# Optimization experiments

Measured on AMD Instinct MI355X. Metric: run time of the kernel, lower is better.

The kernel has to match this reference:

```python
import jax, jax.numpy as jnp
import numpy as np

EPS = 1e-6

def _ln(x, g, b):
    # channels-first LayerNorm over C (per-pixel), matching custom LayerNorm in repo
    m = jnp.mean(x, 1, keepdims=True)
    v = jnp.mean((x - m) ** 2, 1, keepdims=True)
    return (x - m) * jax.lax.rsqrt(v + EPS) * g[None, :, None, None] + b[None, :, None, None]

def _c1(x, w, b=None):
    y = jnp.einsum('oc,bchw->bohw', w, x)
    return y if b is None else y + b[None, :, None, None]

def _dw(x, w, b=None, pad=1, dil=1):
    y = jax.lax.conv_general_dilated(x, w, (1, 1), [(pad, pad), (pad, pad)],
                                     rhs_dilation=(dil, dil), feature_group_count=x.shape[1],
                                     dimension_numbers=('NCHW', 'OIHW', 'NCHW'))
    return y if b is None else y + b[None, :, None, None]

def _dwt_haar(x):
    # single-level 2D haar DWT (zero mode, even H/W so no padding needed)
    a = x[:, :, 0::2, 0::2]; b = x[:, :, 0::2, 1::2]
    c = x[:, :, 1::2, 0::2]; d = x[:, :, 1::2, 1::2]
    ll = (a + b + c + d) * 0.5
    hl = (b - a + d - c) * 0.5
    lh = (c - a + d - b) * 0.5
    hh = (a - b - c + d) * 0.5
    return ll, hl, lh, hh

def _ss2d(x, xp, dtw, dtb, alog, dp):
    # 4-direction Mamba-style selective scan (VMamba SS2D core)
    B, D, H, W = x.shape
    L = H * W; K = 4; R = dtw.shape[-1]; N = alog.shape[-1]
    x1 = x.reshape(B, D, L)                                   # row-major scan
    x2 = jnp.transpose(x, (0, 1, 3, 2)).reshape(B, D, L)      # col-major scan
    xs = jnp.stack([x1, x2], 1)
    xs = jnp.concatenate([xs, jnp.flip(xs, -1)], 1)           # (B,4,D,L)
    xdbl = jnp.einsum('bkdl,kcd->bkcl', xs, xp)               # (B,4,R+2N,L)
    dts, Bs, Cs = jnp.split(xdbl, [R, R + N], axis=2)
    dts = jax.nn.softplus(jnp.einsum('bkrl,kdr->bkdl', dts, dtw) + dtb[None, :, :, None])
    A = -jnp.exp(alog)                                        # (K,D,N)

    def step(h, inp):
        u, dt, Bt, Ct = inp
        h = h * jnp.exp(dt[..., None] * A) + (dt * u)[..., None] * Bt[:, :, None, :]
        return h, jnp.einsum('bkdn,bkn->bkd', h, Ct)

    h0 = jnp.zeros((B, K, D, N), x.dtype)
    _, ys = jax.lax.scan(step, h0, (jnp.moveaxis(xs, -1, 0), jnp.moveaxis(dts, -1, 0),
                                    jnp.moveaxis(Bs, -1, 0), jnp.moveaxis(Cs, -1, 0)))
    y = jnp.moveaxis(ys, 0, -1) + dp[None, :, :, None] * xs   # (B,4,D,L)

    def wh(z):
        return jnp.transpose(z.reshape(B, D, W, H), (0, 1, 3, 2)).reshape(B, D, L)

    out = y[:, 0] + jnp.flip(y[:, 2], -1) + wh(y[:, 1]) + wh(jnp.flip(y[:, 3], -1))
    return out.reshape(B, D, H, W)

def forward(x, wt_dw, wt_db, wt_lng, wt_lnb, wt_ctw, wt_ctb,
            cv_inw, cv_ln1g, cv_ln1b, cv_pw, cv_dww, cv_dwb,
            ss_xp, ss_dtw, ss_dtb, ss_alog, ss_d,
            cv_ong, cv_onb, cv_ow, cv_skip, eca_w, wgm_skip,
            pf_nw, pf_nb, pf_lng, pf_lnb, pf_d1, pf_d2, pf_d3, pf_d4,
            pf_flng, pf_flnb, pf_fw, pf_fb, pf_skip):
    # ---- WT_Block ----
    q = _ln(_c1(x, wt_dw, wt_db), wt_lng, wt_lnb)
    ll, hl, lh, hh = _dwt_haar(q)
    q = jnp.concatenate([ll, hl, lh, hh], 1)                  # (B,C,H/2,W/2)
    # ConvTranspose2d(k=2, s=2): out[2i+p,2j+q] = sum_c in[i,j] * W[c,o,p,q]
    y = jnp.einsum('bcij,copq->boipjq', q, wt_ctw)
    Bq, Co, Hh, _, Ww, _ = y.shape
    q = y.reshape(Bq, Co, 2 * Hh, 2 * Ww) + wt_ctb[None, :, None, None]
    # ---- CVSS_Block ----
    h = _ln(_c1(q, cv_inw), cv_ln1g, cv_ln1b)
    skip_in = h
    h = _c1(h, cv_pw)
    h = jax.nn.silu(_dw(h, cv_dww, cv_dwb, pad=1))
    h = _ss2d(h, ss_xp, ss_dtw, ss_dtb, ss_alog, ss_d)
    h = _ln(h, cv_ong, cv_onb)
    q = _c1(h, cv_ow) + skip_in * cv_skip
    # ---- ECA ----
    v = jnp.mean(q, (2, 3))[:, None, :]                       # (B,1,C)
    v = jax.lax.conv_general_dilated(v, eca_w, (1,), [(1, 1)],
                                     dimension_numbers=('NCH', 'OIH', 'NCH'))
    v = jax.nn.sigmoid(v)[:, 0, :, None, None]
    x = v * q + wgm_skip * x
    # ---- PF_Block ----
    res = _ln(_c1(x, pf_nw, pf_nb), pf_lng, pf_lnb)
    x1, x2, x3, x4 = jnp.split(res, 4, axis=1)
    x1 = _dw(x1, pf_d1, pad=1)
    x2 = _dw(x1 + x2, pf_d2, pad=3)
    x3 = _dw(x2 + x3, pf_d3, pad=2, dil=2)
    x4 = _dw(x3 + x4, pf_d4, pad=3, dil=3)
    cat = jnp.concatenate([x1, x2, x3, x4], 1)
    return jax.nn.silu(_c1(_ln(cat, pf_flng, pf_flnb), pf_fw, pf_fb)) + pf_skip * res

def setup_inputs() -> dict:
    key = jax.random.key(0)
    C, B, H, W = 64, 4, 64, 64
    N, R, D2, K, C4 = 16, 4, 2 * C, 4, C // 4
    ks = jax.random.split(key, 20)
    def rn(i, shape, s):
        return jax.random.normal(ks[i], shape, jnp.float32) * s
    inp = {}
    inp['x'] = jax.random.normal(ks[0], (B, C, H, W), jnp.float32)
    inp['wt_dw'] = rn(1, (C4, C), 0.1); inp['wt_db'] = jnp.zeros((C4,))
    inp['wt_lng'] = jnp.ones((C4,)); inp['wt_lnb'] = jnp.zeros((C4,))
    inp['wt_ctw'] = rn(2, (C, C, 2, 2), 0.1); inp['wt_ctb'] = jnp.zeros((C,))
    inp['cv_inw'] = rn(3, (C, C), 0.1)
    inp['cv_ln1g'] = jnp.ones((C,)); inp['cv_ln1b'] = jnp.zeros((C,))
    inp['cv_pw'] = rn(4, (D2, C), 0.1)
    inp['cv_dww'] = rn(5, (D2, 1, 3, 3), 0.2); inp['cv_dwb'] = jnp.zeros((D2,))
    inp['ss_xp'] = rn(6, (K, R + 2 * N, D2), 0.05)
    inp['ss_dtw'] = rn(7, (K, D2, R), 0.1)
    inp['ss_dtb'] = jnp.full((K, D2), -4.0) + rn(8, (K, D2), 0.1)
    inp['ss_alog'] = jnp.tile(jnp.log(jnp.arange(1.0, N + 1.0, dtype=jnp.float32)), (K, D2, 1))
    inp['ss_d'] = jnp.ones((K, D2))
    inp['cv_ong'] = jnp.ones((D2,)); inp['cv_onb'] = jnp.zeros((D2,))
    inp['cv_ow'] = rn(9, (C, D2), 0.1); inp['cv_skip'] = jnp.ones((1,))
    inp['eca_w'] = rn(10, (1, 1, 3), 0.5)
    inp['wgm_skip'] = jnp.ones((1,))
    inp['pf_nw'] = rn(11, (C, C), 0.1); inp['pf_nb'] = jnp.zeros((C,))
    inp['pf_lng'] = jnp.ones((C,)); inp['pf_lnb'] = jnp.zeros((C,))
    inp['pf_d1'] = rn(12, (C4, 1, 3, 3), 0.2)
    inp['pf_d2'] = rn(13, (C4, 1, 7, 7), 0.1)
    inp['pf_d3'] = rn(14, (C4, 1, 3, 3), 0.2)
    inp['pf_d4'] = rn(15, (C4, 1, 3, 3), 0.2)
    inp['pf_flng'] = jnp.ones((C,)); inp['pf_flnb'] = jnp.zeros((C,))
    inp['pf_fw'] = rn(16, (C, C), 0.1); inp['pf_fb'] = jnp.zeros((C,))
    inp['pf_skip'] = jnp.ones((1,))
    return inp

def reference(x, wt_dw, wt_db, wt_lng, wt_lnb, wt_ctw, wt_ctb,
              cv_inw, cv_ln1g, cv_ln1b, cv_pw, cv_dww, cv_dwb,
              ss_xp, ss_dtw, ss_dtb, ss_alog, ss_d,
              cv_ong, cv_onb, cv_ow, cv_skip, eca_w, wgm_skip,
              pf_nw, pf_nb, pf_lng, pf_lnb, pf_d1, pf_d2, pf_d3, pf_d4,
              pf_flng, pf_flnb, pf_fw, pf_fb, pf_skip):
    return forward(x, wt_dw, wt_db, wt_lng, wt_lnb, wt_ctw, wt_ctb,
                   cv_inw, cv_ln1g, cv_ln1b, cv_pw, cv_dww, cv_dwb,
                   ss_xp, ss_dtw, ss_dtb, ss_alog, ss_d,
                   cv_ong, cv_onb, cv_ow, cv_skip, eca_w, wgm_skip,
                   pf_nw, pf_nb, pf_lng, pf_lnb, pf_d1, pf_d2, pf_d3, pf_d4,
                   pf_flng, pf_flnb, pf_fw, pf_fb, pf_skip)
```

## Files before the change

kernel.cpp:

```cpp
#include <hip/hip_runtime.h>
#include <cstdint>
#include <cstddef>

#define B_ 4
#define C_ 64
#define C4_ 16
#define D_ 128
#define H_ 64
#define W_ 64
#define L_ 4096
#define K_ 4
#define N_ 16
#define R_ 4
#define NC_ 64
#define CL_ 64
#define EPS_ 1e-6f

#define DEV __device__ __forceinline__

DEV float sigmoidf_(float x){ return 1.f/(1.f+__expf(-x)); }
DEV float siluf_(float x){ return x*sigmoidf_(x); }
DEV float softplusf_(float x){ return fmaxf(x,0.f) + __logf(1.f+__expf(-fabsf(x))); }

__global__ __launch_bounds__(64) void k1_inln(
    const float* __restrict__ x, const float* __restrict__ w,
    const float* __restrict__ bias, const float* __restrict__ g,
    const float* __restrict__ bb, float* __restrict__ q1)
{
  int t = blockIdx.x*64 + threadIdx.x;
  int b = t >> 12; int pix = t & (L_-1);
  const float* xb = x + (size_t)b*C_*L_ + pix;
  float acc[C4_];
  #pragma unroll
  for(int o=0;o<C4_;o++) acc[o] = bias[o];
  for(int c=0;c<C_;c++){
    float xv = xb[(size_t)c*L_];
    #pragma unroll
    for(int o=0;o<C4_;o++) acc[o] = fmaf(w[o*C_+c], xv, acc[o]);
  }
  float m=0.f;
  #pragma unroll
  for(int o=0;o<C4_;o++) m += acc[o];
  m *= (1.f/C4_);
  float var=0.f;
  #pragma unroll
  for(int o=0;o<C4_;o++){ float d=acc[o]-m; var += d*d; }
  var *= (1.f/C4_);
  float rs = rsqrtf(var+EPS_);
  float* qb = q1 + (size_t)b*C4_*L_ + pix;
  #pragma unroll
  for(int o=0;o<C4_;o++) qb[(size_t)o*L_] = (acc[o]-m)*rs*g[o] + bb[o];
}

__global__ __launch_bounds__(256) void k2a_dwtct(
    const float* __restrict__ q1, const float* __restrict__ ctw,
    const float* __restrict__ ctb, float* __restrict__ q2)
{
  int t = blockIdx.x*256 + threadIdx.x;
  int pix = t & (L_-1);
  int bq = t >> 12; int b = bq >> 2; int quarter = bq & 3;
  int y = pix >> 6, xw = pix & 63;
  int i = y >> 1, p = y & 1, j = xw >> 1, q = xw & 1;
  const float* qb = q1 + (size_t)b*C4_*L_;
  int p00 = (2*i)*W_ + 2*j;
  float ll[16], hl[16], lh[16], hh[16];
  #pragma unroll
  for(int c=0;c<16;c++){
    const float* pc = qb + (size_t)c*L_ + p00;
    float a = pc[0], bb2 = pc[1], cc = pc[W_], dd = pc[W_+1];
    ll[c] = (a+bb2+cc+dd)*0.5f;
    hl[c] = (bb2-a+dd-cc)*0.5f;
    lh[c] = (cc-a+dd-bb2)*0.5f;
    hh[c] = (a-bb2-cc+dd)*0.5f;
  }
  int pq = p*2+q;
  int obase = quarter*16;
  float* q2b = q2 + (size_t)b*C_*L_ + pix;
  #pragma unroll
  for(int oo=0;oo<16;oo++){
    int o = obase+oo;
    float acc = ctb[o];
    const float* wb = ctw + o*4 + pq;
    #pragma unroll
    for(int c=0;c<16;c++){
      acc = fmaf(ll[c], wb[c*256],       acc);
      acc = fmaf(hl[c], wb[(16+c)*256],  acc);
      acc = fmaf(lh[c], wb[(32+c)*256],  acc);
      acc = fmaf(hh[c], wb[(48+c)*256],  acc);
    }
    q2b[(size_t)o*L_] = acc;
  }
}

__global__ __launch_bounds__(64) void k2b_inconv_ln(
    const float* __restrict__ q2, const float* __restrict__ w,
    const float* __restrict__ g, const float* __restrict__ bb,
    float* __restrict__ skip)
{
  int t = blockIdx.x*64 + threadIdx.x;
  int b = t >> 12; int pix = t & (L_-1);
  const float* qb = q2 + (size_t)b*C_*L_ + pix;
  float acc[C_];
  #pragma unroll
  for(int o=0;o<C_;o++) acc[o]=0.f;
  for(int c=0;c<C_;c++){
    float xv = qb[(size_t)c*L_];
    #pragma unroll
    for(int o=0;o<C_;o++) acc[o] = fmaf(w[o*C_+c], xv, acc[o]);
  }
  float m=0.f;
  #pragma unroll
  for(int o=0;o<C_;o++) m += acc[o];
  m *= (1.f/C_);
  float var=0.f;
  #pragma unroll
  for(int o=0;o<C_;o++){ float d=acc[o]-m; var += d*d; }
  var *= (1.f/C_);
  float rs = rsqrtf(var+EPS_);
  float* sb = skip + (size_t)b*C_*L_ + pix;
  #pragma unroll
  for(int o=0;o<C_;o++) sb[(size_t)o*L_] = (acc[o]-m)*rs*g[o] + bb[o];
}

__global__ __launch_bounds__(256) void k3_pw(
    const float* __restrict__ skip, const float* __restrict__ w,
    float* __restrict__ hp)
{
  int t = blockIdx.x*256 + threadIdx.x;
  int pix = t & (L_-1);
  int bg = t >> 12; int b = bg >> 3; int grp = bg & 7;
  const float* sb = skip + (size_t)b*C_*L_ + pix;
  float acc[16];
  #pragma unroll
  for(int o=0;o<16;o++) acc[o]=0.f;
  for(int c=0;c<C_;c++){
    float xv = sb[(size_t)c*L_];
    #pragma unroll
    for(int oo=0;oo<16;oo++) acc[oo]=fmaf(w[(grp*16+oo)*C_+c], xv, acc[oo]);
  }
  float* hb = hp + (size_t)b*D_*L_ + (size_t)(grp*16)*L_ + pix;
  #pragma unroll
  for(int oo=0;oo<16;oo++) hb[(size_t)oo*L_] = acc[oo];
}

__global__ __launch_bounds__(256) void k4_dwsilu(
    const float* __restrict__ hp, const float* __restrict__ wdw,
    const float* __restrict__ bdw, float* __restrict__ hd,
    float* __restrict__ hdt)
{
  __shared__ float tin[64][65];
  __shared__ float tout[64][65];
  int bc = blockIdx.x;
  int ch = bc & (D_-1);
  const float* plane = hp + (size_t)bc*L_;
  int tid = threadIdx.x;
  #pragma unroll
  for(int qq=0;qq<16;qq++){ int lin = tid + qq*256; tin[lin>>6][lin&63] = plane[lin]; }
  __syncthreads();
  float wv[9];
  #pragma unroll
  for(int i=0;i<9;i++) wv[i] = wdw[ch*9+i];
  float bv = bdw[ch];
  float* hdp = hd + (size_t)bc*L_;
  #pragma unroll
  for(int qq=0;qq<16;qq++){
    int lin = tid + qq*256; int h = lin>>6, w = lin&63;
    float acc = bv;
    #pragma unroll
    for(int ky=0;ky<3;ky++){
      int hh = h+ky-1; if(hh<0||hh>=64) continue;
      #pragma unroll
      for(int kx=0;kx<3;kx++){
        int ww = w+kx-1; if(ww<0||ww>=64) continue;
        acc = fmaf(wv[ky*3+kx], tin[hh][ww], acc);
      }
    }
    float s = siluf_(acc);
    hdp[lin] = s;
    tout[h][w] = s;
  }
  __syncthreads();
  float* hdtp = hdt + (size_t)bc*L_;
  #pragma unroll
  for(int qq=0;qq<16;qq++){
    int lin = tid + qq*256;
    hdtp[lin] = tout[lin&63][lin>>6];
  }
}

__global__ __launch_bounds__(256) void k5_proj(
    const float* __restrict__ hd, const float* __restrict__ hdt,
    const float* __restrict__ xp, float* __restrict__ xd4,
    float* __restrict__ bsb, float* __restrict__ csb)
{
  int l = blockIdx.x*256 + threadIdx.x;
  int k = blockIdx.y, b = blockIdx.z;
  int pixv = (k<2)? l : (L_-1-l);
  const float* src = ((k&1)? hdt : hd) + (size_t)b*D_*L_ + pixv;
  const float* xpk = xp + k*36*D_;
  float xd[36];
  #pragma unroll
  for(int c=0;c<36;c++) xd[c]=0.f;
  for(int d=0;d<D_;d++){
    float u = src[(size_t)d*L_];
    #pragma unroll
    for(int c=0;c<36;c++) xd[c] = fmaf(xpk[c*D_+d], u, xd[c]);
  }
  int bk = b*K_+k;
  float4* xq = (float4*)(xd4 + ((size_t)bk*L_ + l)*4);
  *xq = make_float4(xd[0], xd[1], xd[2], xd[3]);
  float* bp = bsb + ((size_t)bk*L_ + l)*N_;
  float* cp = csb + ((size_t)bk*L_ + l)*N_;
  #pragma unroll
  for(int n=0;n<N_;n++){ bp[n]=xd[4+n]; cp[n]=xd[20+n]; }
}


__global__ __launch_bounds__(128) void k6_scan1(
    const float* __restrict__ xd4, const float* __restrict__ hd,
    const float* __restrict__ hdt, const float* __restrict__ bsb,
    const float* __restrict__ dtw, const float* __restrict__ dtb,
    const float* __restrict__ alog, float* __restrict__ ca, float* __restrict__ cb)
{
  __shared__ float su[128][65];
  __shared__ float4 sb4[64][4];
  __shared__ float4 sx[64];
  int chunk = blockIdx.x, k = blockIdx.y, b = blockIdx.z;
  int d = threadIdx.x;
  int bk = b*K_ + k;
  bool rev = (k >= 2);
  int base_l = rev ? (63-chunk)*CL_ : chunk*CL_;
  const float* src = ((k&1)? hdt : hd) + (size_t)b*D_*L_;
  #pragma unroll
  for(int p=0;p<16;p++){
    int idx = p*128 + d; int row = idx >> 4, c4 = idx & 15;
    float4 v = *(const float4*)(src + (size_t)row*L_ + base_l + c4*4);
    su[row][c4*4+0]=v.x; su[row][c4*4+1]=v.y; su[row][c4*4+2]=v.z; su[row][c4*4+3]=v.w;
  }
  const float4* bsrc = (const float4*)(bsb + ((size_t)bk*L_ + chunk*CL_)*N_);
  #pragma unroll
  for(int p=0;p<2;p++){
    int idx = p*128 + d; int row = idx>>2, q = idx&3;
    sb4[row][q] = bsrc[idx];
  }
  {
    const float4* xsrc = (const float4*)(xd4 + ((size_t)bk*L_ + chunk*CL_)*4);
    if(d < 64) sx[d] = xsrc[d];
  }
  float A[N_];
  {
    const float* al = alog + ((size_t)k*D_+d)*N_;
    #pragma unroll
    for(int n=0;n<N_;n++) A[n] = -__expf(al[n]);
  }
  float4 wv = *(const float4*)(dtw + ((size_t)k*D_+d)*R_);
  float bdt = dtb[k*D_+d];
  __syncthreads();
  float h[N_];
  #pragma unroll
  for(int n=0;n<N_;n++) h[n]=0.f;
  float S=0.f;
  for(int i=0;i<CL_;i++){
    int jj = rev ? (CL_-1-i) : i;
    float4 xv = sx[i];
    float r = fmaf(xv.x,wv.x, fmaf(xv.y,wv.y, fmaf(xv.z,wv.z, fmaf(xv.w,wv.w, bdt))));
    float dt = softplusf_(r);
    float u = su[d][jj];
    S += dt;
    float du = dt*u;
    #pragma unroll
    for(int n4=0;n4<4;n4++){
      float4 bv = sb4[i][n4];
      int n0=n4*4;
      h[n0+0] = fmaf(du, bv.x, h[n0+0]*__expf(dt*A[n0+0]));
      h[n0+1] = fmaf(du, bv.y, h[n0+1]*__expf(dt*A[n0+1]));
      h[n0+2] = fmaf(du, bv.z, h[n0+2]*__expf(dt*A[n0+2]));
      h[n0+3] = fmaf(du, bv.w, h[n0+3]*__expf(dt*A[n0+3]));
    }
  }
  size_t obase = (((size_t)bk*NC_ + chunk)*D_ + d)*N_;
  float4* cap = (float4*)(ca + obase);
  float4* cbp = (float4*)(cb + obase);
  #pragma unroll
  for(int n4=0;n4<4;n4++){
    int n0=n4*4;
    cap[n4] = make_float4(__expf(S*A[n0]), __expf(S*A[n0+1]), __expf(S*A[n0+2]), __expf(S*A[n0+3]));
    cbp[n4] = make_float4(h[n0], h[n0+1], h[n0+2], h[n0+3]);
  }
}

__global__ __launch_bounds__(256) void k7_scan2(
    const float* __restrict__ ca, const float* __restrict__ cb,
    float* __restrict__ h0)
{
  int t = blockIdx.x*256 + threadIdx.x;
  int bk = t >> 11; int dn = t & 2047;
  size_t base = (size_t)bk*NC_*D_*N_ + dn;
  float h=0.f;
  for(int c=0;c<NC_;c++){
    size_t idx = base + (size_t)c*D_*N_;
    h0[idx] = h;
    h = fmaf(ca[idx], h, cb[idx]);
  }
}

__global__ __launch_bounds__(128) void k8_scan3(
    const float* __restrict__ xd4, const float* __restrict__ hd,
    const float* __restrict__ hdt, const float* __restrict__ bsb,
    const float* __restrict__ csb, const float* __restrict__ h0b,
    const float* __restrict__ dtw, const float* __restrict__ dtb,
    const float* __restrict__ alog, const float* __restrict__ dp,
    float* __restrict__ ys)
{
  __shared__ float su[128][65];
  __shared__ float4 sb4[64][4];
  __shared__ float4 sc4[64][4];
  __shared__ float4 sx[64];
  int chunk = blockIdx.x, k = blockIdx.y, b = blockIdx.z;
  int d = threadIdx.x;
  int bk = b*K_ + k;
  bool rev = (k >= 2);
  int base_l = rev ? (63-chunk)*CL_ : chunk*CL_;
  const float* src = ((k&1)? hdt : hd) + (size_t)b*D_*L_;
  #pragma unroll
  for(int p=0;p<16;p++){
    int idx = p*128 + d; int row = idx >> 4, c4 = idx & 15;
    float4 v = *(const float4*)(src + (size_t)row*L_ + base_l + c4*4);
    su[row][c4*4+0]=v.x; su[row][c4*4+1]=v.y; su[row][c4*4+2]=v.z; su[row][c4*4+3]=v.w;
  }
  const float4* bsrc = (const float4*)(bsb + ((size_t)bk*L_ + chunk*CL_)*N_);
  const float4* csrc = (const float4*)(csb + ((size_t)bk*L_ + chunk*CL_)*N_);
  #pragma unroll
  for(int p=0;p<2;p++){
    int idx = p*128 + d; int row = idx>>2, q = idx&3;
    sb4[row][q] = bsrc[idx];
    sc4[row][q] = csrc[idx];
  }
  {
    const float4* xsrc = (const float4*)(xd4 + ((size_t)bk*L_ + chunk*CL_)*4);
    if(d < 64) sx[d] = xsrc[d];
  }
  float A[N_];
  {
    const float* al = alog + ((size_t)k*D_+d)*N_;
    #pragma unroll
    for(int n=0;n<N_;n++) A[n] = -__expf(al[n]);
  }
  float4 wv = *(const float4*)(dtw + ((size_t)k*D_+d)*R_);
  float bdt = dtb[k*D_+d];
  float dpv = dp[k*D_+d];
  float h[N_];
  {
    size_t hbase = (((size_t)bk*NC_ + chunk)*D_ + d)*N_;
    const float4* h4 = (const float4*)(h0b + hbase);
    #pragma unroll
    for(int n4=0;n4<4;n4++){
      float4 hv = h4[n4];
      h[n4*4+0]=hv.x; h[n4*4+1]=hv.y; h[n4*4+2]=hv.z; h[n4*4+3]=hv.w;
    }
  }
  __syncthreads();
  for(int i=0;i<CL_;i++){
    int jj = rev ? (CL_-1-i) : i;
    float4 xv = sx[i];
    float r = fmaf(xv.x,wv.x, fmaf(xv.y,wv.y, fmaf(xv.z,wv.z, fmaf(xv.w,wv.w, bdt))));
    float dt = softplusf_(r);
    float u = su[d][jj];
    float du = dt*u;
    float y = 0.f;
    #pragma unroll
    for(int n4=0;n4<4;n4++){
      float4 bv = sb4[i][n4];
      float4 cv = sc4[i][n4];
      int n0=n4*4;
      h[n0+0] = fmaf(du, bv.x, h[n0+0]*__expf(dt*A[n0+0])); y = fmaf(h[n0+0], cv.x, y);
      h[n0+1] = fmaf(du, bv.y, h[n0+1]*__expf(dt*A[n0+1])); y = fmaf(h[n0+1], cv.y, y);
      h[n0+2] = fmaf(du, bv.z, h[n0+2]*__expf(dt*A[n0+2])); y = fmaf(h[n0+2], cv.z, y);
      h[n0+3] = fmaf(du, bv.w, h[n0+3]*__expf(dt*A[n0+3])); y = fmaf(h[n0+3], cv.w, y);
    }
    y = fmaf(dpv, u, y);
    su[d][jj] = y;
  }
  __syncthreads();
  #pragma unroll
  for(int p=0;p<16;p++){
    int idx = p*128 + d; int row = idx >> 4, c4 = idx & 15;
    int m0 = c4*4;
    float4 v;
    if(rev) v = make_float4(su[row][63-m0], su[row][62-m0], su[row][61-m0], su[row][60-m0]);
    else    v = make_float4(su[row][m0], su[row][m0+1], su[row][m0+2], su[row][m0+3]);
    *(float4*)(ys + ((size_t)bk*D_ + row)*L_ + chunk*CL_ + m0) = v;
  }
}

__global__ __launch_bounds__(256) void k9t_comb(
    const float* __restrict__ ys, float* __restrict__ yc)
{
  __shared__ float t1[64][65];
  __shared__ float t3[64][65];
  int bd = blockIdx.x; int b = bd >> 7; int d = bd & (D_-1);
  const float* y0 = ys + ((size_t)(b*K_+0)*D_ + d)*L_;
  const float* y1 = ys + ((size_t)(b*K_+1)*D_ + d)*L_;
  const float* y2 = ys + ((size_t)(b*K_+2)*D_ + d)*L_;
  const float* y3 = ys + ((size_t)(b*K_+3)*D_ + d)*L_;
  int tid = threadIdx.x;
  #pragma unroll
  for(int qq=0;qq<16;qq++){
    int lin = tid + qq*256;
    t1[lin>>6][lin&63] = y1[lin];
    t3[lin>>6][lin&63] = y3[lin];
  }
  __syncthreads();
  float* outp = yc + ((size_t)b*D_ + d)*L_;
  #pragma unroll
  for(int qq=0;qq<16;qq++){
    int lin = tid + qq*256; int h = lin>>6, w = lin&63;
    outp[lin] = y0[lin] + t1[w][h] + y2[L_-1-lin] + t3[63-w][63-h];
  }
}

__global__ __launch_bounds__(256) void k9a_ln(
    const float* __restrict__ yc, const float* __restrict__ g,
    const float* __restrict__ bb, float* __restrict__ hn)
{
  __shared__ float ssum[4][64];
  __shared__ float ssq[4][64];
  int tid = threadIdx.x;
  int pl = tid & 63;
  int wg = tid >> 6;
  int t = blockIdx.x*64 + pl;
  int b = t >> 12; int pix = t & (L_-1);
  const float* ybase = yc + (size_t)b*D_*L_ + (size_t)(wg*32)*L_ + pix;
  float v[32];
  float s = 0.f;
  #pragma unroll
  for(int i=0;i<32;i++){ v[i] = ybase[(size_t)i*L_]; s += v[i]; }
  ssum[wg][pl] = s;
  __syncthreads();
  float S = ssum[0][pl]+ssum[1][pl]+ssum[2][pl]+ssum[3][pl];
  float m = S*(1.f/D_);
  float vq = 0.f;
  #pragma unroll
  for(int i=0;i<32;i++){ float dv = v[i]-m; vq = fmaf(dv,dv,vq); }
  ssq[wg][pl] = vq;
  __syncthreads();
  float VQ = ssq[0][pl]+ssq[1][pl]+ssq[2][pl]+ssq[3][pl];
  float rs = rsqrtf(VQ*(1.f/D_)+EPS_);
  float* hb = hn + (size_t)b*D_*L_ + (size_t)(wg*32)*L_ + pix;
  #pragma unroll
  for(int i=0;i<32;i++) hb[(size_t)i*L_] = (v[i]-m)*rs*g[wg*32+i] + bb[wg*32+i];
}

__global__ __launch_bounds__(256) void k9b_ow(
    const float* __restrict__ hn, const float* __restrict__ w,
    const float* __restrict__ skip, const float* __restrict__ cskip,
    float* __restrict__ qg, float* __restrict__ meansum)
{
  int t = blockIdx.x*256 + threadIdx.x;
  int pix = t & (L_-1); int bg = t >> 12; int b = bg >> 2; int grp = bg & 3;
  const float* hb = hn + (size_t)b*D_*L_ + pix;
  float acc[16];
  #pragma unroll
  for(int o=0;o<16;o++) acc[o]=0.f;
  for(int dd=0;dd<D_;dd++){
    float xv = hb[(size_t)dd*L_];
    #pragma unroll
    for(int oo=0;oo<16;oo++) acc[oo]=fmaf(w[(grp*16+oo)*D_+dd], xv, acc[oo]);
  }
  float csk = cskip[0];
  const float* sb = skip + (size_t)b*C_*L_ + pix;
  float* qb = qg + (size_t)b*C_*L_ + pix;
  #pragma unroll
  for(int oo=0;oo<16;oo++){
    int o = grp*16+oo;
    float v = acc[oo] + csk*sb[(size_t)o*L_];
    qb[(size_t)o*L_] = v;
    acc[oo] = v;
  }
  #pragma unroll
  for(int oo=0;oo<16;oo++){
    float v = acc[oo];
    #pragma unroll
    for(int off=32;off>0;off>>=1) v += __shfl_down(v, off, 64);
    if((threadIdx.x & 63)==0) atomicAdd(&meansum[b*C_ + grp*16+oo], v);
  }
}

__global__ __launch_bounds__(256) void k10_eca(
    const float* __restrict__ meansum, const float* __restrict__ ew,
    float* __restrict__ vsig)
{
  int t = threadIdx.x; if(t >= B_*C_) return;
  int b=t>>6, c=t&63;
  const float sc = 1.f/(float)L_;
  float ml = (c>0)?  meansum[b*C_+c-1]*sc : 0.f;
  float mc =         meansum[b*C_+c]*sc;
  float mr = (c<63)? meansum[b*C_+c+1]*sc : 0.f;
  float r = ew[0]*ml + ew[1]*mc + ew[2]*mr;
  vsig[t] = sigmoidf_(r);
}

__global__ __launch_bounds__(64) void k11_res(
    const float* __restrict__ qg, const float* __restrict__ xin,
    const float* __restrict__ vsig, const float* __restrict__ wgm,
    const float* __restrict__ w, const float* __restrict__ nb,
    const float* __restrict__ g, const float* __restrict__ bb,
    float* __restrict__ res)
{
  int t = blockIdx.x*64 + threadIdx.x;
  int b = t >> 12, pix = t & (L_-1);
  float wg = wgm[0];
  const float* qb = qg + (size_t)b*C_*L_ + pix;
  const float* xb = xin + (size_t)b*C_*L_ + pix;
  float acc[C_];
  #pragma unroll
  for(int o=0;o<C_;o++) acc[o]=nb[o];
  for(int c=0;c<C_;c++){
    float x2 = vsig[b*C_+c]*qb[(size_t)c*L_] + wg*xb[(size_t)c*L_];
    #pragma unroll
    for(int o=0;o<C_;o++) acc[o] = fmaf(w[o*C_+c], x2, acc[o]);
  }
  float m=0.f;
  #pragma unroll
  for(int o=0;o<C_;o++) m += acc[o];
  m *= (1.f/C_);
  float var=0.f;
  #pragma unroll
  for(int o=0;o<C_;o++){ float d=acc[o]-m; var += d*d; }
  var *= (1.f/C_);
  float rs = rsqrtf(var+EPS_);
  float* rb = res + (size_t)b*C_*L_ + pix;
  #pragma unroll
  for(int o=0;o<C_;o++) rb[(size_t)o*L_] = (acc[o]-m)*rs*g[o] + bb[o];
}

DEV void conv_step(const float (*tin)[65], float (*tout)[65],
                   const float* __restrict__ wp, int ks, int pad, int dil,
                   float* __restrict__ gout, int tid)
{
  for(int qq=0;qq<16;qq++){
    int lin=tid+qq*256; int h=lin>>6, w=lin&63;
    float acc=0.f;
    for(int ky=0;ky<ks;ky++){
      int hh=h+ky*dil-pad; if(hh<0||hh>=64) continue;
      for(int kx=0;kx<ks;kx++){
        int ww=w+kx*dil-pad; if(ww<0||ww>=64) continue;
        acc = fmaf(wp[ky*ks+kx], tin[hh][ww], acc);
      }
    }
    tout[h][w]=acc; gout[lin]=acc;
  }
}

__global__ __launch_bounds__(256) void k12_cascade(
    const float* __restrict__ res, const float* __restrict__ d1,
    const float* __restrict__ d2, const float* __restrict__ d3,
    const float* __restrict__ d4, float* __restrict__ cat)
{
  __shared__ float ta[64][65];
  __shared__ float tb[64][65];
  int bc = blockIdx.x; int b = bc>>4; int c = bc&15;
  int tid = threadIdx.x;
  const float* rb = res + (size_t)b*C_*L_;
  float* catb = cat + (size_t)b*C_*L_;
  for(int qq=0;qq<16;qq++){ int lin=tid+qq*256; ta[lin>>6][lin&63] = rb[(size_t)c*L_+lin]; }
  __syncthreads();
  conv_step(ta, tb, d1+c*9, 3, 1, 1, catb + (size_t)c*L_, tid);
  __syncthreads();
  for(int qq=0;qq<16;qq++){ int lin=tid+qq*256; ta[lin>>6][lin&63] = tb[lin>>6][lin&63] + rb[(size_t)(16+c)*L_+lin]; }
  __syncthreads();
  conv_step(ta, tb, d2+c*49, 7, 3, 1, catb + (size_t)(16+c)*L_, tid);
  __syncthreads();
  for(int qq=0;qq<16;qq++){ int lin=tid+qq*256; ta[lin>>6][lin&63] = tb[lin>>6][lin&63] + rb[(size_t)(32+c)*L_+lin]; }
  __syncthreads();
  conv_step(ta, tb, d3+c*9, 3, 2, 2, catb + (size_t)(32+c)*L_, tid);
  __syncthreads();
  for(int qq=0;qq<16;qq++){ int lin=tid+qq*256; ta[lin>>6][lin&63] = tb[lin>>6][lin&63] + rb[(size_t)(48+c)*L_+lin]; }
  __syncthreads();
  conv_step(ta, tb, d4+c*9, 3, 3, 3, catb + (size_t)(48+c)*L_, tid);
}

__global__ __launch_bounds__(64) void k13_final(
    const float* __restrict__ cat, const float* __restrict__ res,
    const float* __restrict__ g, const float* __restrict__ bb,
    const float* __restrict__ fw, const float* __restrict__ fb,
    const float* __restrict__ pskip, float* __restrict__ out)
{
  int t = blockIdx.x*64 + threadIdx.x;
  int b = t >> 12, pix = t & (L_-1);
  const float* catb = cat + (size_t)b*C_*L_ + pix;
  float s=0.f;
  for(int c=0;c<C_;c++) s += catb[(size_t)c*L_];
  float m = s*(1.f/C_);
  float var=0.f;
  for(int c=0;c<C_;c++){ float d=catb[(size_t)c*L_]-m; var += d*d; }
  var *= (1.f/C_);
  float rs = rsqrtf(var+EPS_);
  float acc[C_];
  #pragma unroll
  for(int o=0;o<C_;o++) acc[o]=fb[o];
  for(int c=0;c<C_;c++){
    float cv = (catb[(size_t)c*L_]-m)*rs*g[c]+bb[c];
    #pragma unroll
    for(int o=0;o<C_;o++) acc[o] = fmaf(fw[o*C_+c], cv, acc[o]);
  }
  float ps = pskip[0];
  const float* rb = res + (size_t)b*C_*L_ + pix;
  float* ob = out + (size_t)b*C_*L_ + pix;
  #pragma unroll
  for(int o=0;o<C_;o++) ob[(size_t)o*L_] = siluf_(acc[o]) + ps*rb[(size_t)o*L_];
}

extern "C" void kernel_launch(void* const* d_in, const int* in_sizes, int n_in,
                              void* d_out, int out_size, void* d_ws, size_t ws_size,
                              hipStream_t stream)
{
  const float* x       = (const float*)d_in[0];
  const float* wt_dw   = (const float*)d_in[1];
  const float* wt_db   = (const float*)d_in[2];
  const float* wt_lng  = (const float*)d_in[3];
  const float* wt_lnb  = (const float*)d_in[4];
  const float* wt_ctw  = (const float*)d_in[5];
  const float* wt_ctb  = (const float*)d_in[6];
  const float* cv_inw  = (const float*)d_in[7];
  const float* cv_ln1g = (const float*)d_in[8];
  const float* cv_ln1b = (const float*)d_in[9];
  const float* cv_pw   = (const float*)d_in[10];
  const float* cv_dww  = (const float*)d_in[11];
  const float* cv_dwb  = (const float*)d_in[12];
  const float* ss_xp   = (const float*)d_in[13];
  const float* ss_dtw  = (const float*)d_in[14];
  const float* ss_dtb  = (const float*)d_in[15];
  const float* ss_alog = (const float*)d_in[16];
  const float* ss_d    = (const float*)d_in[17];
  const float* cv_ong  = (const float*)d_in[18];
  const float* cv_onb  = (const float*)d_in[19];
  const float* cv_ow   = (const float*)d_in[20];
  const float* cv_skip = (const float*)d_in[21];
  const float* eca_w   = (const float*)d_in[22];
  const float* wgm_skip= (const float*)d_in[23];
  const float* pf_nw   = (const float*)d_in[24];
  const float* pf_nb   = (const float*)d_in[25];
  const float* pf_lng  = (const float*)d_in[26];
  const float* pf_lnb  = (const float*)d_in[27];
  const float* pf_d1   = (const float*)d_in[28];
  const float* pf_d2   = (const float*)d_in[29];
  const float* pf_d3   = (const float*)d_in[30];
  const float* pf_d4   = (const float*)d_in[31];
  const float* pf_flng = (const float*)d_in[32];
  const float* pf_flnb = (const float*)d_in[33];
  const float* pf_fw   = (const float*)d_in[34];
  const float* pf_fb   = (const float*)d_in[35];
  const float* pf_skip = (const float*)d_in[36];
  float* outp = (float*)d_out;

  float* ws = (float*)d_ws;
  size_t off = 0;
  float* q1   = ws+off; off += (size_t)B_*C4_*L_;
  float* q2   = ws+off;
  float* qg   = q2;
  off += (size_t)B_*C_*L_;
  float* skip = ws+off; off += (size_t)B_*C_*L_;
  float* hp   = ws+off;
  float* ca   = hp;
  off += (size_t)B_*D_*L_;
  float* hd   = ws+off;
  float* res  = hd;
  off += (size_t)B_*D_*L_;
  float* hdt  = ws+off;
  float* cat  = hdt;
  off += (size_t)B_*D_*L_;
  float* xd4  = ws+off; off += (size_t)B_*K_*L_*R_;
  float* bs   = ws+off; off += (size_t)B_*K_*L_*N_;
  float* cs   = ws+off; off += (size_t)B_*K_*L_*N_;
  float* cb   = ws+off;
  float* hn   = cb;
  off += (size_t)B_*K_*D_*NC_*N_;
  float* h0   = ws+off;
  float* yc   = h0;
  off += (size_t)B_*K_*D_*NC_*N_;
  float* ys   = ws+off; off += (size_t)B_*K_*D_*L_;
  float* meansum = ws+off; off += 256;
  float* vsig    = ws+off; off += 256;
  (void)ws_size; (void)in_sizes; (void)n_in; (void)out_size;

  hipMemsetAsync(meansum, 0, B_*C_*sizeof(float), stream);

  k1_inln   <<<256, 64, 0, stream>>>(x, wt_dw, wt_db, wt_lng, wt_lnb, q1);
  k2a_dwtct <<<256, 256, 0, stream>>>(q1, wt_ctw, wt_ctb, q2);
  k2b_inconv_ln<<<256, 64, 0, stream>>>(q2, cv_inw, cv_ln1g, cv_ln1b, skip);
  k3_pw     <<<512, 256, 0, stream>>>(skip, cv_pw, hp);
  k4_dwsilu <<<512, 256, 0, stream>>>(hp, cv_dww, cv_dwb, hd, hdt);
  k5_proj   <<<dim3(16,4,4), 256, 0, stream>>>(hd, hdt, ss_xp, xd4, bs, cs);
  k6_scan1  <<<dim3(NC_,K_,B_), 128, 0, stream>>>(xd4, hd, hdt, bs, ss_dtw, ss_dtb, ss_alog, ca, cb);
  k7_scan2  <<<128, 256, 0, stream>>>(ca, cb, h0);
  k8_scan3  <<<dim3(NC_,K_,B_), 128, 0, stream>>>(xd4, hd, hdt, bs, cs, h0, ss_dtw, ss_dtb, ss_alog, ss_d, ys);
  k9t_comb  <<<512, 256, 0, stream>>>(ys, yc);
  k9a_ln    <<<256, 256, 0, stream>>>(yc, cv_ong, cv_onb, hn);
  k9b_ow    <<<256, 256, 0, stream>>>(hn, cv_ow, skip, cv_skip, qg, meansum);
  k10_eca   <<<1,   256, 0, stream>>>(meansum, eca_w, vsig);
  k11_res   <<<256, 64, 0, stream>>>(qg, x, vsig, wgm_skip, pf_nw, pf_nb, pf_lng, pf_lnb, res);
  k12_cascade<<<64, 256, 0, stream>>>(res, pf_d1, pf_d2, pf_d3, pf_d4, cat);
  k13_final <<<256, 64, 0, stream>>>(cat, res, pf_flng, pf_flnb, pf_fw, pf_fb, pf_skip, outp);
}
```

Before: 614.0 us.

## Split 64-channel pointwise+LN kernels across 4 warps and stage DWT weights in LDS

```diff
diff --git a/kernel.cpp b/kernel.cpp
--- a/kernel.cpp
+++ b/kernel.cpp
@@ -56,70 +56,90 @@
     const float* __restrict__ q1, const float* __restrict__ ctw,
     const float* __restrict__ ctb, float* __restrict__ q2)
 {
-  int t = blockIdx.x*256 + threadIdx.x;
-  int pix = t & (L_-1);
-  int bq = t >> 12; int b = bq >> 2; int quarter = bq & 3;
+  __shared__ float wl[4][64][16];
+  int blk = blockIdx.x;
+  int bq = blk >> 4; int b = bq >> 2; int quarter = bq & 3;
+  int tid = threadIdx.x;
+  #pragma unroll
+  for(int pp=0;pp<16;pp++){
+    int v = pp*256 + tid;
+    int pq = v >> 10; int c = (v >> 4) & 63; int o = v & 15;
+    wl[pq][c][o] = ctw[c*256 + (quarter*16+o)*4 + pq];
+  }
+  __syncthreads();
+  int pix = ((blk & 15) << 8) + tid;
   int y = pix >> 6, xw = pix & 63;
   int i = y >> 1, p = y & 1, j = xw >> 1, q = xw & 1;
+  int pq = p*2+q;
   const float* qb = q1 + (size_t)b*C4_*L_;
   int p00 = (2*i)*W_ + 2*j;
-  float ll[16], hl[16], lh[16], hh[16];
+  float acc[16];
+  #pragma unroll
+  for(int oo=0;oo<16;oo++) acc[oo] = ctb[quarter*16+oo];
   #pragma unroll
   for(int c=0;c<16;c++){
     const float* pc = qb + (size_t)c*L_ + p00;
     float a = pc[0], bb2 = pc[1], cc = pc[W_], dd = pc[W_+1];
-    ll[c] = (a+bb2+cc+dd)*0.5f;
-    hl[c] = (bb2-a+dd-cc)*0.5f;
-    lh[c] = (cc-a+dd-bb2)*0.5f;
-    hh[c] = (a-bb2-cc+dd)*0.5f;
-  }
-  int pq = p*2+q;
-  int obase = quarter*16;
-  float* q2b = q2 + (size_t)b*C_*L_ + pix;
-  #pragma unroll
-  for(int oo=0;oo<16;oo++){
-    int o = obase+oo;
-    float acc = ctb[o];
-    const float* wb = ctw + o*4 + pq;
-    #pragma unroll
-    for(int c=0;c<16;c++){
-      acc = fmaf(ll[c], wb[c*256],       acc);
-      acc = fmaf(hl[c], wb[(16+c)*256],  acc);
-      acc = fmaf(lh[c], wb[(32+c)*256],  acc);
-      acc = fmaf(hh[c], wb[(48+c)*256],  acc);
+    float ll = (a+bb2+cc+dd)*0.5f;
+    float hl = (bb2-a+dd-cc)*0.5f;
+    float lh = (cc-a+dd-bb2)*0.5f;
+    float hh = (a-bb2-cc+dd)*0.5f;
+    const float4* wll = (const float4*)&wl[pq][c][0];
+    const float4* whl = (const float4*)&wl[pq][16+c][0];
+    const float4* wlh = (const float4*)&wl[pq][32+c][0];
+    const float4* whh = (const float4*)&wl[pq][48+c][0];
+    #pragma unroll
+    for(int o4=0;o4<4;o4++){
+      float4 w0 = wll[o4], w1 = whl[o4], w2 = wlh[o4], w3 = whh[o4];
+      int o0 = o4*4;
+      acc[o0+0] = fmaf(ll,w0.x, fmaf(hl,w1.x, fmaf(lh,w2.x, fmaf(hh,w3.x, acc[o0+0]))));
+      acc[o0+1] = fmaf(ll,w0.y, fmaf(hl,w1.y, fmaf(lh,w2.y, fmaf(hh,w3.y, acc[o0+1]))));
+      acc[o0+2] = fmaf(ll,w0.z, fmaf(hl,w1.z, fmaf(lh,w2.z, fmaf(hh,w3.z, acc[o0+2]))));
+      acc[o0+3] = fmaf(ll,w0.w, fmaf(hl,w1.w, fmaf(lh,w2.w, fmaf(hh,w3.w, acc[o0+3]))));
     }
-    q2b[(size_t)o*L_] = acc;
-  }
-}
-
-__global__ __launch_bounds__(64) void k2b_inconv_ln(
+  }
+  float* q2b = q2 + (size_t)b*C_*L_ + (size_t)(quarter*16)*L_ + pix;
+  #pragma unroll
+  for(int oo=0;oo<16;oo++) q2b[(size_t)oo*L_] = acc[oo];
+}
+
+__global__ __launch_bounds__(256) void k2b_inconv_ln(
     const float* __restrict__ q2, const float* __restrict__ w,
     const float* __restrict__ g, const float* __restrict__ bb,
     float* __restrict__ skip)
 {
-  int t = blockIdx.x*64 + threadIdx.x;
+  __shared__ float ssum[4][64];
+  __shared__ float ssq[4][64];
+  int tid = threadIdx.x;
+  int pl = tid & 63, wg = tid >> 6;
+  int t = blockIdx.x*64 + pl;
   int b = t >> 12; int pix = t & (L_-1);
   const float* qb = q2 + (size_t)b*C_*L_ + pix;
-  float acc[C_];
-  #pragma unroll
-  for(int o=0;o<C_;o++) acc[o]=0.f;
+  const float* wrow = w + wg*16*C_;
+  float acc[16];
+  #pragma unroll
+  for(int o=0;o<16;o++) acc[o]=0.f;
   for(int c=0;c<C_;c++){
     float xv = qb[(size_t)c*L_];
     #pragma unroll
-    for(int o=0;o<C_;o++) acc[o] = fmaf(w[o*C_+c], xv, acc[o]);
-  }
-  float m=0.f;
-  #pragma unroll
-  for(int o=0;o<C_;o++) m += acc[o];
-  m *= (1.f/C_);
-  float var=0.f;
-  #pragma unroll
-  for(int o=0;o<C_;o++){ float d=acc[o]-m; var += d*d; }
-  var *= (1.f/C_);
+    for(int o=0;o<16;o++) acc[o] = fmaf(wrow[o*C_+c], xv, acc[o]);
+  }
+  float s=0.f;
+  #pragma unroll
+  for(int o=0;o<16;o++) s += acc[o];
+  ssum[wg][pl] = s;
+  __syncthreads();
+  float m = (ssum[0][pl]+ssum[1][pl]+ssum[2][pl]+ssum[3][pl])*(1.f/C_);
+  float vq=0.f;
+  #pragma unroll
+  for(int o=0;o<16;o++){ float d=acc[o]-m; vq = fmaf(d,d,vq); }
+  ssq[wg][pl] = vq;
+  __syncthreads();
+  float var = (ssq[0][pl]+ssq[1][pl]+ssq[2][pl]+ssq[3][pl])*(1.f/C_);
   float rs = rsqrtf(var+EPS_);
-  float* sb = skip + (size_t)b*C_*L_ + pix;
-  #pragma unroll
-  for(int o=0;o<C_;o++) sb[(size_t)o*L_] = (acc[o]-m)*rs*g[o] + bb[o];
+  float* sb = skip + (size_t)b*C_*L_ + (size_t)(wg*16)*L_ + pix;
+  #pragma unroll
+  for(int o=0;o<16;o++) sb[(size_t)o*L_] = (acc[o]-m)*rs*g[wg*16+o] + bb[wg*16+o];
 }
 
 __global__ __launch_bounds__(256) void k3_pw(
@@ -500,38 +520,47 @@
   vsig[t] = sigmoidf_(r);
 }
 
-__global__ __launch_bounds__(64) void k11_res(
+__global__ __launch_bounds__(256) void k11_res(
     const float* __restrict__ qg, const float* __restrict__ xin,
     const float* __restrict__ vsig, const float* __restrict__ wgm,
     const float* __restrict__ w, const float* __restrict__ nb,
     const float* __restrict__ g, const float* __restrict__ bb,
     float* __restrict__ res)
 {
-  int t = blockIdx.x*64 + threadIdx.x;
-  int b = t >> 12, pix = t & (L_-1);
-  float wg = wgm[0];
+  __shared__ float ssum[4][64];
+  __shared__ float ssq[4][64];
+  int tid = threadIdx.x;
+  int pl = tid & 63, wg2 = tid >> 6;
+  int t = blockIdx.x*64 + pl;
+  int b = t >> 12; int pix = t & (L_-1);
+  float wgs = wgm[0];
   const float* qb = qg + (size_t)b*C_*L_ + pix;
   const float* xb = xin + (size_t)b*C_*L_ + pix;
-  float acc[C_];
-  #pragma unroll
-  for(int o=0;o<C_;o++) acc[o]=nb[o];
+  const float* wrow = w + wg2*16*C_;
+  float acc[16];
+  #pragma unroll
+  for(int o=0;o<16;o++) acc[o]=nb[wg2*16+o];
   for(int c=0;c<C_;c++){
-    float x2 = vsig[b*C_+c]*qb[(size_t)c*L_] + wg*xb[(size_t)c*L_];
-    #pragma unroll
-    for(int o=0;o<C_;o++) acc[o] = fmaf(w[o*C_+c], x2, acc[o]);
-  }
-  float m=0.f;
-  #pragma unroll
-  for(int o=0;o<C_;o++) m += acc[o];
-  m *= (1.f/C_);
-  float var=0.f;
-  #pragma unroll
-  for(int o=0;o<C_;o++){ float d=acc[o]-m; var += d*d; }
-  var *= (1.f/C_);
+    float x2 = vsig[b*C_+c]*qb[(size_t)c*L_] + wgs*xb[(size_t)c*L_];
+    #pragma unroll
+    for(int o=0;o<16;o++) acc[o] = fmaf(wrow[o*C_+c], x2, acc[o]);
+  }
+  float s=0.f;
+  #pragma unroll
+  for(int o=0;o<16;o++) s += acc[o];
+  ssum[wg2][pl] = s;
+  __syncthreads();
+  float m = (ssum[0][pl]+ssum[1][pl]+ssum[2][pl]+ssum[3][pl])*(1.f/C_);
+  float vq=0.f;
+  #pragma unroll
+  for(int o=0;o<16;o++){ float d=acc[o]-m; vq = fmaf(d,d,vq); }
+  ssq[wg2][pl] = vq;
+  __syncthreads();
+  float var = (ssq[0][pl]+ssq[1][pl]+ssq[2][pl]+ssq[3][pl])*(1.f/C_);
   float rs = rsqrtf(var+EPS_);
-  float* rb = res + (size_t)b*C_*L_ + pix;
-  #pragma unroll
-  for(int o=0;o<C_;o++) rb[(size_t)o*L_] = (acc[o]-m)*rs*g[o] + bb[o];
+  float* rb = res + (size_t)b*C_*L_ + (size_t)(wg2*16)*L_ + pix;
+  #pragma unroll
+  for(int o=0;o<16;o++) rb[(size_t)o*L_] = (acc[o]-m)*rs*g[wg2*16+o] + bb[wg2*16+o];
 }
 
 DEV void conv_step(const float (*tin)[65], float (*tout)[65],
@@ -580,35 +609,40 @@
   conv_step(ta, tb, d4+c*9, 3, 3, 3, catb + (size_t)(48+c)*L_, tid);
 }
 
-__global__ __launch_bounds__(64) void k13_final(
+__global__ __launch_bounds__(256) void k13_final(
     const float* __restrict__ cat, const float* __restrict__ res,
     const float* __restrict__ g, const float* __restrict__ bb,
     const float* __restrict__ fw, const float* __restrict__ fb,
     const float* __restrict__ pskip, float* __restrict__ out)
 {
-  int t = blockIdx.x*64 + threadIdx.x;
-  int b = t >> 12, pix = t & (L_-1);
+  int t = blockIdx.x*256 + threadIdx.x;
+  int pix = t & (L_-1); int bg = t >> 12; int b = bg >> 2; int grp = bg & 3;
   const float* catb = cat + (size_t)b*C_*L_ + pix;
+  float cv[C_];
   float s=0.f;
-  for(int c=0;c<C_;c++) s += catb[(size_t)c*L_];
+  #pragma unroll
+  for(int c=0;c<C_;c++){ cv[c] = catb[(size_t)c*L_]; s += cv[c]; }
   float m = s*(1.f/C_);
   float var=0.f;
-  for(int c=0;c<C_;c++){ float d=catb[(size_t)c*L_]-m; var += d*d; }
+  #pragma unroll
+  for(int c=0;c<C_;c++){ float d=cv[c]-m; var = fmaf(d,d,var); }
   var *= (1.f/C_);
   float rs = rsqrtf(var+EPS_);
-  float acc[C_];
-  #pragma unroll
-  for(int o=0;o<C_;o++) acc[o]=fb[o];
+  const float* wrow = fw + grp*16*C_;
+  float acc[16];
+  #pragma unroll
+  for(int o=0;o<16;o++) acc[o]=fb[grp*16+o];
+  #pragma unroll
   for(int c=0;c<C_;c++){
-    float cv = (catb[(size_t)c*L_]-m)*rs*g[c]+bb[c];
-    #pragma unroll
-    for(int o=0;o<C_;o++) acc[o] = fmaf(fw[o*C_+c], cv, acc[o]);
+    float nv = (cv[c]-m)*rs*g[c]+bb[c];
+    #pragma unroll
+    for(int o=0;o<16;o++) acc[o] = fmaf(wrow[o*C_+c], nv, acc[o]);
   }
   float ps = pskip[0];
-  const float* rb = res + (size_t)b*C_*L_ + pix;
-  float* ob = out + (size_t)b*C_*L_ + pix;
-  #pragma unroll
-  for(int o=0;o<C_;o++) ob[(size_t)o*L_] = siluf_(acc[o]) + ps*rb[(size_t)o*L_];
+  const float* rb = res + (size_t)b*C_*L_ + (size_t)(grp*16)*L_ + pix;
+  float* ob = out + (size_t)b*C_*L_ + (size_t)(grp*16)*L_ + pix;
+  #pragma unroll
+  for(int o=0;o<16;o++) ob[(size_t)o*L_] = siluf_(acc[o]) + ps*rb[(size_t)o*L_];
 }
 
 extern "C" void kernel_launch(void* const* d_in, const int* in_sizes, int n_in,
@@ -688,7 +722,7 @@
 
   k1_inln   <<<256, 64, 0, stream>>>(x, wt_dw, wt_db, wt_lng, wt_lnb, q1);
   k2a_dwtct <<<256, 256, 0, stream>>>(q1, wt_ctw, wt_ctb, q2);
-  k2b_inconv_ln<<<256, 64, 0, stream>>>(q2, cv_inw, cv_ln1g, cv_ln1b, skip);
+  k2b_inconv_ln<<<256, 256, 0, stream>>>(q2, cv_inw, cv_ln1g, cv_ln1b, skip);
   k3_pw     <<<512, 256, 0, stream>>>(skip, cv_pw, hp);
   k4_dwsilu <<<512, 256, 0, stream>>>(hp, cv_dww, cv_dwb, hd, hdt);
   k5_proj   <<<dim3(16,4,4), 256, 0, stream>>>(hd, hdt, ss_xp, xd4, bs, cs);
@@ -699,7 +733,7 @@
   k9a_ln    <<<256, 256, 0, stream>>>(yc, cv_ong, cv_onb, hn);
   k9b_ow    <<<256, 256, 0, stream>>>(hn, cv_ow, skip, cv_skip, qg, meansum);
   k10_eca   <<<1,   256, 0, stream>>>(meansum, eca_w, vsig);
-  k11_res   <<<256, 64, 0, stream>>>(qg, x, vsig, wgm_skip, pf_nw, pf_nb, pf_lng, pf_lnb, res);
+  k11_res   <<<256, 256, 0, stream>>>(qg, x, vsig, wgm_skip, pf_nw, pf_nb, pf_lng, pf_lnb, res);
   k12_cascade<<<64, 256, 0, stream>>>(res, pf_d1, pf_d2, pf_d3, pf_d4, cat);
-  k13_final <<<256, 64, 0, stream>>>(cat, res, pf_flng, pf_flnb, pf_fw, pf_fb, pf_skip, outp);
-}
+  k13_final <<<256, 256, 0, stream>>>(cat, res, pf_flng, pf_flnb, pf_fw, pf_fb, pf_skip, outp);
+}
```

Result: faster. 527.0 us (-14.2%).
